# Performance work log

Measured on AMD Instinct MI355X. Metric: run time of the kernel, lower is better.

## Reference

```python
import jax, jax.numpy as jnp
import numpy as np

N_ATOMS = 30000
N_PAIRS = 1200000
N_BASIS = 7
N_RADIAL = 5
N_SPECIES = 119
R_MIN = 0.5
R_MAX = 6.0
UNITS = (512, 512)
BOX = 6.0  # Angstrom box edge so many pairs fall inside the cutoff
N_FEAT = 360  # gaussian-moment feature count for n_radial=5

# static triangular index sets (fully symmetric contractions)
_TRI2_I, _TRI2_J = np.triu_indices(N_RADIAL)
_TRI3 = np.array([(i, j, k) for i in range(N_RADIAL)
                  for j in range(i, N_RADIAL)
                  for k in range(j, N_RADIAL)], dtype=np.int32)


def setup_inputs() -> dict:
    key = jax.random.key(0)
    ks = jax.random.split(key, 8)
    R = jax.random.uniform(ks[0], (N_ATOMS, 3), jnp.float32) * BOX
    Z = jax.random.randint(ks[1], (N_ATOMS,), 0, N_SPECIES, dtype=jnp.int32)
    idx = jax.random.randint(ks[2], (2, N_PAIRS), 0, N_ATOMS, dtype=jnp.int32)
    W_radial = jax.random.normal(ks[3], (N_SPECIES, N_SPECIES, N_RADIAL, N_BASIS), jnp.float32) / np.sqrt(N_BASIS)
    w1 = jax.random.normal(ks[4], (N_FEAT, UNITS[0]), jnp.float32) / np.sqrt(N_FEAT)
    b1 = jnp.zeros((UNITS[0],), jnp.float32)
    w2 = jax.random.normal(ks[5], (UNITS[0], UNITS[1]), jnp.float32) / np.sqrt(UNITS[0])
    b2 = jnp.zeros((UNITS[1],), jnp.float32)
    w3 = jax.random.normal(ks[6], (UNITS[1], 1), jnp.float32) / np.sqrt(UNITS[1])
    b3 = jnp.zeros((1,), jnp.float32)
    scale = 2.0 * jnp.ones((N_SPECIES, 1), jnp.float32)
    shift = 1.0 * jnp.ones((N_SPECIES, 1), jnp.float32)
    return dict(R=R, Z=Z, idx=idx, W_radial=W_radial, w1=w1, b1=b1,
                w2=w2, b2=b2, w3=w3, b3=b3, scale=scale, shift=shift)


def _descriptor(R, Z, idx, W_radial):
    idx_i, idx_j = idx[0], idx[1]
    # pairwise displacement (free-space displacement fn)
    dr_vec = R[idx_j] - R[idx_i]                                  # [P,3]
    dr = jnp.sqrt(jnp.sum(dr_vec * dr_vec, axis=-1) + 1e-12)      # [P]
    dn = dr_vec / (dr + 1e-5)[:, None]                            # unit vectors [P,3]

    # gaussian radial basis
    betta = N_BASIS ** 2 / R_MAX ** 2
    rad_norm = (2.0 * betta / np.pi) ** 0.25
    shifts = R_MIN + (R_MAX - R_MIN) / N_BASIS * jnp.arange(N_BASIS, dtype=jnp.float32)
    basis = rad_norm * jnp.exp(-betta * (dr[:, None] - shifts) ** 2)  # [P,B]

    # cosine cutoff and per species-pair embedding of the basis
    cutoff = 0.5 * (jnp.cos(jnp.pi * dr / R_MAX) + 1.0) * (dr < R_MAX)
    coeffs = W_radial[Z[idx_i], Z[idx_j]]                          # [P,K,B] irregular gather
    radial = jnp.einsum('pkb,pb->pk', coeffs, basis)               # [P,K]
    radial = radial * (cutoff / np.sqrt(N_BASIS))[:, None]

    seg = lambda x: jax.ops.segment_sum(x, idx_i, num_segments=N_ATOMS)
    # geometric moments of order 0..3
    m0 = seg(radial)                                               # [A,K]
    m1 = seg(radial[:, :, None] * dn[:, None, :])                  # [A,K,3]
    dn2 = dn[:, :, None] * dn[:, None, :]                          # [P,3,3]
    m2 = seg(radial[:, :, None, None] * dn2[:, None])              # [A,K,3,3]
    dn3 = dn2[:, :, :, None] * dn[:, None, None, :]                # [P,3,3,3]
    m3 = seg(radial[:, :, None, None, None] * dn3[:, None])        # [A,K,3,3,3]

    # gaussian-moment invariant contractions
    c1 = jnp.einsum('ari,asi->ars', m1, m1)
    c2 = jnp.einsum('arij,asij->ars', m2, m2)
    c3 = jnp.einsum('arijk,asijk->ars', m3, m3)
    c4 = jnp.einsum('arij,asik,atjk->arst', m2, m2, m2)
    c5 = jnp.einsum('ari,asj,atij->arst', m1, m1, m2)
    c6 = jnp.einsum('arijk,asijl,atkl->arst', m3, m3, m2)
    c7 = jnp.einsum('arijk,asij,atk->arst', m3, m2, m1)

    A = m0.shape[0]
    gm = jnp.concatenate([
        m0,
        c1[:, _TRI2_I, _TRI2_J],
        c2[:, _TRI2_I, _TRI2_J],
        c3[:, _TRI2_I, _TRI2_J],
        c4[:, _TRI3[:, 0], _TRI3[:, 1], _TRI3[:, 2]],
        c5[:, _TRI2_I, _TRI2_J, :].reshape(A, -1),
        c6[:, _TRI2_I, _TRI2_J, :].reshape(A, -1),
        c7.reshape(A, -1),
    ], axis=-1)                                                    # [A,360]
    return gm


def reference(R, Z, idx, W_radial, w1, b1, w2, b2, w3, b3, scale, shift):
    gm = _descriptor(R, Z, idx, W_radial)
    h = jax.nn.swish(gm @ w1 + b1)
    h = jax.nn.swish(h @ w2 + b2)
    h = h @ w3 + b3                                                # [A,1]
    return scale[Z] * h + shift[Z]
```

## Files before the change

kernel.cpp:

```cpp
#include <hip/hip_runtime.h>

#define NA      30000
#define MPAD    30080
#define NPAIRS  1200000
#define NB      7
#define NK      5
#define NSP     119
#define NFEAT   360
#define KP1     384
#define NU      512
#define WROW    36
#define MAXSLOT 120
#define PSTRIDE 128
#define NBK     118
#define BCAP    11520
#define PPB     4688
#define NTILE   235

#define BETTA      1.3611111111111112f
#define RADNORM    0.96481348f
#define SHIFT_STEP 0.7857142857142857f
#define PI_OVER_R  0.5235987755982988f
#define INV_SQRT7  0.3779644730092272f
#define RMAXV      6.0f

typedef __attribute__((ext_vector_type(8))) short bf16x8;
typedef __attribute__((ext_vector_type(4))) float f32x4;
typedef __attribute__((ext_vector_type(2))) float f32x2;

__device__ __forceinline__ unsigned short f2b(float x) {
    unsigned u = __float_as_uint(x);
    unsigned r = u + 0x7FFF + ((u >> 16) & 1);
    return (unsigned short)(r >> 16);
}

__global__ __launch_bounds__(256)
void k_part(const int* __restrict__ idx, const int* __restrict__ Z,
            int* __restrict__ gcur, int* __restrict__ part) {
    __shared__ int hist[NBK];
    __shared__ int base[NBK];
    int tid = threadIdx.x;
    for (int b = tid; b < NBK; b += 256) hist[b] = 0;
    __syncthreads();
    int p0 = blockIdx.x * PPB;
    int p1 = min(p0 + PPB, NPAIRS);
    for (int p = p0 + tid; p < p1; p += 256)
        atomicAdd(&hist[idx[p] >> 8], 1);
    __syncthreads();
    for (int b = tid; b < NBK; b += 256) {
        base[b] = atomicAdd(&gcur[b], hist[b]);
        hist[b] = 0;
    }
    __syncthreads();
    for (int p = p0 + tid; p < p1; p += 256) {
        int i = idx[p];
        int b = i >> 8;
        int j = idx[NPAIRS + p];
        int zj = Z[j];
        int off = base[b] + atomicAdd(&hist[b], 1);
        if (off < BCAP)
            part[b * BCAP + off] = ((i & 255) << 22) | (zj << 15) | j;
    }
}

__global__ __launch_bounds__(256)
void k_csr(const int* __restrict__ part, const int* __restrict__ gcnt,
           int* __restrict__ counts, int* __restrict__ plist) {
    __shared__ int lp[128 * MAXSLOT];
    __shared__ int lc[128];
    int tid = threadIdx.x;
    int lane = tid & 63, wave = tid >> 6;
    int w = blockIdx.x;
    int cb = w >> 1;
    int par = w & 1;
    for (int t = tid; t < 128; t += 256) lc[t] = 0;
    __syncthreads();
    int n = min(gcnt[cb], BCAP);
    for (int e = tid; e < n; e += 256) {
        int v = part[cb * BCAP + e];
        int iloc = v >> 22;
        if ((iloc >> 7) == par) {
            int i7 = iloc & 127;
            int r = atomicAdd(&lc[i7], 1);
            if (r < MAXSLOT) lp[i7 * MAXSLOT + r] = v & 0x3FFFFF;
        }
    }
    __syncthreads();
    for (int t = tid; t < 128; t += 256) {
        int a = w * 128 + t;
        if (a < NA) counts[a] = min(lc[t], MAXSLOT);
    }
    for (int rr = 0; rr < 32; rr++) {
        int row = wave * 32 + rr;
        int a = w * 128 + row;
        if (a < NA) {
            for (int c = lane; c < MAXSLOT; c += 64)
                plist[(size_t)a * PSTRIDE + c] = lp[row * MAXSLOT + c];
        }
    }
}

#define PREP_W   (NSP*NSP*WROW)
#define PREP_R   NA
#define PREP_W1  (NU*KP1)
#define PREP_W2  (NU*NU)
#define PREP_TOT (PREP_W + PREP_R + PREP_W1 + PREP_W2)
__global__ void k_prep(const float* __restrict__ W, const float* __restrict__ R,
                       const float* __restrict__ w1, const float* __restrict__ w2,
                       float* __restrict__ Wp, float* __restrict__ Rp,
                       unsigned short* __restrict__ w1T, unsigned short* __restrict__ w2T,
                       int* __restrict__ gcur, float* __restrict__ out) {
    int i = blockIdx.x * blockDim.x + threadIdx.x;
    if (i < 128) gcur[i] = 0;
    if (i < NA) out[i] = 0.f;
    if (i < PREP_W) {
        int row = i / WROW, e = i - row * WROW;
        Wp[i] = (e < NK * NB) ? W[row * (NK * NB) + e] : 0.f;
        return;
    }
    i -= PREP_W;
    if (i < PREP_R) {
        f32x4 v = {R[3*i], R[3*i+1], R[3*i+2], 0.f};
        *(f32x4*)&Rp[4*i] = v;
        return;
    }
    i -= PREP_R;
    if (i < PREP_W1) {
        int c = i / KP1, kp = i - c * KP1;
        w1T[i] = (kp < NFEAT) ? f2b(w1[kp * NU + c]) : (unsigned short)0;
        return;
    }
    i -= PREP_W1;
    if (i < PREP_W2) {
        int c = i >> 9, kp = i & 511;
        w2T[i] = f2b(w2[kp * NU + c]);
    }
}

__global__ __launch_bounds__(512, 2)
void k_momcon(const float* __restrict__ Rp, const int* __restrict__ Z,
              const float* __restrict__ Wp, const int* __restrict__ counts,
              const int* __restrict__ plist, unsigned short* __restrict__ gmB) {
    __shared__ float MS[100 * 65];
    int tid = threadIdx.x;
    int g = tid >> 3, q = tid & 7;
    int a0 = blockIdx.x * 64;
    int a = a0 + g;

    if (a < NA) {
        f32x4 ri = *(const f32x4*)&Rp[4*a];
        int Zi = Z[a];
        f32x2 acc[50];
#pragma unroll
        for (int u = 0; u < 50; u++) acc[u] = (f32x2){0.f, 0.f};
        int cnt = min(counts[a], MAXSLOT);
        const int* prow = plist + (size_t)a * PSTRIDE;

        for (int t = q; t < cnt; t += 8) {
            int pk = prow[t];
            int j  = pk & 0x7FFF;
            int Zj = (pk >> 15) & 0x7F;
            f32x4 rj = *(const f32x4*)&Rp[4*j];

            const f32x4* wrow = (const f32x4*)&Wp[(Zi * NSP + Zj) * WROW];
            f32x4 w4[9];
#pragma unroll
            for (int c = 0; c < 9; c++) w4[c] = wrow[c];
            const float* wf = (const float*)w4;

            float dx = rj.x - ri.x, dy = rj.y - ri.y, dz = rj.z - ri.z;
            float d2 = dx*dx + dy*dy + dz*dz + 1e-12f;
            float dr = sqrtf(d2);
            float inv = 1.0f / (dr + 1e-5f);
            float nx = dx*inv, ny = dy*inv, nz = dz*inv;

            float basis[NB];
#pragma unroll
            for (int b = 0; b < NB; b++) {
                float tt = dr - (0.5f + SHIFT_STEP * (float)b);
                basis[b] = RADNORM * __expf(-BETTA * tt * tt);
            }
            float cut = (dr < RMAXV) ? 0.5f * (__cosf(PI_OVER_R * dr) + 1.0f) : 0.0f;
            cut *= INV_SQRT7;
            float rad[NK];
#pragma unroll
            for (int k = 0; k < NK; k++) {
                float s = 0.f;
#pragma unroll
                for (int b = 0; b < NB; b++) s += wf[k*NB + b] * basis[b];
                rad[k] = s * cut;
            }
            float gg[20];
            gg[0] = 1.f; gg[1] = nx; gg[2] = ny; gg[3] = nz;
            gg[4] = nx*nx; gg[5] = nx*ny; gg[6] = nx*nz; gg[7] = ny*ny; gg[8] = ny*nz; gg[9] = nz*nz;
            gg[10] = gg[4]*nx; gg[11] = gg[4]*ny; gg[12] = gg[4]*nz; gg[13] = gg[5]*ny; gg[14] = gg[5]*nz;
            gg[15] = gg[6]*nz; gg[16] = gg[7]*ny; gg[17] = gg[7]*nz; gg[18] = gg[8]*nz; gg[19] = gg[9]*nz;
            f32x2 g2[10];
#pragma unroll
            for (int u = 0; u < 10; u++) g2[u] = (f32x2){gg[2*u], gg[2*u+1]};
#pragma unroll
            for (int k = 0; k < NK; k++) {
                f32x2 rk = (f32x2){rad[k], rad[k]};
#pragma unroll
                for (int u = 0; u < 10; u++)
                    acc[k*10 + u] += rk * g2[u];
            }
        }
#pragma unroll
        for (int u = 0; u < 50; u++) {
            f32x2 v = acc[u];
            double d = __builtin_bit_cast(double, v);
            d = __shfl_xor(d, 1);
            v += __builtin_bit_cast(f32x2, d);
            d = __builtin_bit_cast(double, v);
            d = __shfl_xor(d, 2);
            v += __builtin_bit_cast(f32x2, d);
            d = __builtin_bit_cast(double, v);
            d = __shfl_xor(d, 4);
            v += __builtin_bit_cast(f32x2, d);
            acc[u] = v;
        }
        if (q == 0) {
#pragma unroll
            for (int u = 0; u < 50; u++) {
                MS[(2*u)     * 65 + g] = acc[u].x;
                MS[(2*u + 1) * 65 + g] = acc[u].y;
            }
        }
    }
    __syncthreads();

    int lane = tid & 63, wave = tid >> 6;
    if (wave >= 4) return;
    int aB = a0 + lane;
    bool ok = (aB < NA);
    const int S2[3][3] = {{0,1,2},{1,3,4},{2,4,5}};
    const int S3[3][3][3] = {
        {{0,1,2},{1,3,4},{2,4,5}},
        {{1,3,4},{3,6,7},{4,7,8}},
        {{2,4,5},{4,7,8},{5,8,9}}
    };
    unsigned short* row = gmB + (size_t)aB * KP1;
#define LD(comp) MS[(comp) * 65 + lane]

    if (wave == 0) {
        if (ok) {
            for (int k = 0; k < 5; k++) row[k] = f2b(LD(k * 20));
        }
        int f = 5;
        for (int r = 0; r < 5; r++)
            for (int s = r; s < 5; s++) {
                float v = 0.f;
#pragma unroll
                for (int i = 0; i < 3; i++) v += LD(r*20+1+i) * LD(s*20+1+i);
                if (ok) row[f] = f2b(v);
                f++;
            }
        const float W2U[6] = {1,2,2,1,2,1};
        for (int r = 0; r < 5; r++)
            for (int s = r; s < 5; s++) {
                float v = 0.f;
#pragma unroll
                for (int u = 0; u < 6; u++) v += W2U[u] * LD(r*20+4+u) * LD(s*20+4+u);
                if (ok) row[f] = f2b(v);
                f++;
            }
        const float W3U[10] = {1,3,3,3,6,3,1,3,3,1};
        for (int r = 0; r < 5; r++)
            for (int s = r; s < 5; s++) {
                float v = 0.f;
#pragma unroll
                for (int u = 0; u < 10; u++) v += W3U[u] * LD(r*20+10+u) * LD(s*20+10+u);
                if (ok) row[f] = f2b(v);
                f++;
            }
        for (int r = 0; r < 5; r++) {
            float m2r[6];
#pragma unroll
            for (int u = 0; u < 6; u++) m2r[u] = LD(r*20+4+u);
            for (int s = r; s < 5; s++) {
                float m2q[6];
#pragma unroll
                for (int u = 0; u < 6; u++) m2q[u] = LD(s*20+4+u);
                for (int t = s; t < 5; t++) {
                    float m2t[6];
#pragma unroll
                    for (int u = 0; u < 6; u++) m2t[u] = LD(t*20+4+u);
                    float v = 0.f;
#pragma unroll
                    for (int i = 0; i < 3; i++)
#pragma unroll
                        for (int j = 0; j < 3; j++)
#pragma unroll
                            for (int k = 0; k < 3; k++)
                                v += m2r[S2[i][j]] * m2q[S2[i][k]] * m2t[S2[j][k]];
                    if (ok) row[f] = f2b(v);
                    f++;
                }
            }
        }
    } else if (wave == 1) {
        int f = 85;
        for (int r = 0; r < 5; r++) {
            float m1r[3];
#pragma unroll
            for (int i = 0; i < 3; i++) m1r[i] = LD(r*20+1+i);
            for (int s = r; s < 5; s++) {
                float m1q[3];
#pragma unroll
                for (int i = 0; i < 3; i++) m1q[i] = LD(s*20+1+i);
                for (int t = 0; t < 5; t++) {
                    float m2t[6];
#pragma unroll
                    for (int u = 0; u < 6; u++) m2t[u] = LD(t*20+4+u);
                    float v = 0.f;
#pragma unroll
                    for (int i = 0; i < 3; i++)
#pragma unroll
                        for (int j = 0; j < 3; j++)
                            v += m1r[i] * m1q[j] * m2t[S2[i][j]];
                    if (ok) row[f] = f2b(v);
                    f++;
                }
            }
        }
        f = 235;
        for (int r = 0; r < 5; r++) {
            float m3r[10];
#pragma unroll
            for (int u = 0; u < 10; u++) m3r[u] = LD(r*20+10+u);
            for (int s = 0; s < 5; s++) {
                float m2q[6];
#pragma unroll
                for (int u = 0; u < 6; u++) m2q[u] = LD(s*20+4+u);
                float U0 = 0.f, U1 = 0.f, U2 = 0.f;
#pragma unroll
                for (int i = 0; i < 3; i++)
#pragma unroll
                    for (int j = 0; j < 3; j++) {
                        float ww = m2q[S2[i][j]];
                        U0 += m3r[S3[i][j][0]] * ww;
                        U1 += m3r[S3[i][j][1]] * ww;
                        U2 += m3r[S3[i][j][2]] * ww;
                    }
                for (int t = 0; t < 5; t++) {
                    float v = U0 * LD(t*20+1) + U1 * LD(t*20+2) + U2 * LD(t*20+3);
                    if (ok) row[f] = f2b(v);
                    f++;
                }
            }
        }
    } else {
        int pbeg = (wave == 2) ? 0 : 7;
        int pend = (wave == 2) ? 7 : 15;
        int p = 0;
        for (int r = 0; r < 5; r++)
            for (int s = r; s < 5; s++) {
                if (p >= pbeg && p < pend) {
                    float m3r[10], m3q[10];
#pragma unroll
                    for (int u = 0; u < 10; u++) m3r[u] = LD(r*20+10+u);
#pragma unroll
                    for (int u = 0; u < 10; u++) m3q[u] = LD(s*20+10+u);
                    float T[3][3];
#pragma unroll
                    for (int k = 0; k < 3; k++)
#pragma unroll
                        for (int l = 0; l < 3; l++) {
                            float v = 0.f;
#pragma unroll
                            for (int i = 0; i < 3; i++)
#pragma unroll
                                for (int j = 0; j < 3; j++)
                                    v += m3r[S3[i][j][k]] * m3q[S3[i][j][l]];
                            T[k][l] = v;
                        }
                    int f = 160 + p * 5;
                    for (int t = 0; t < 5; t++) {
                        float m2t[6];
#pragma unroll
                        for (int u = 0; u < 6; u++) m2t[u] = LD(t*20+4+u);
                        float v = 0.f;
#pragma unroll
                        for (int k = 0; k < 3; k++)
#pragma unroll
                            for (int l = 0; l < 3; l++)
                                v += T[k][l] * m2t[S2[k][l]];
                        if (ok) row[f + t] = f2b(v);
                    }
                }
                p++;
            }
        if (wave == 3 && ok) {
            for (int z = NFEAT; z < KP1; z++) row[z] = 0;
        }
    }
#undef LD
}

__device__ __forceinline__ void stage8(const unsigned short* gp, unsigned short* lp) {
    __builtin_amdgcn_global_load_lds(
        (const __attribute__((address_space(1))) unsigned int*)gp,
        (__attribute__((address_space(3))) unsigned int*)lp, 16, 0, 0);
}

template<int KPAD, int MODE>
__global__ __launch_bounds__(256) void k_mfma(const unsigned short* __restrict__ A,
                                              const unsigned short* __restrict__ B,
                                              const float* __restrict__ bias,
                                              const float* __restrict__ w3,
                                              void* __restrict__ outp) {
    __shared__ __align__(16) unsigned char SMEM[35072];
    unsigned short* As = (unsigned short*)SMEM;
    unsigned short* Bs = (unsigned short*)(SMEM + 16384);
    float* red = (float*)(SMEM + 32768);
    int tid = threadIdx.x;
    int lane = tid & 63, wave = tid >> 6;
    int wm = wave >> 1, wn = wave & 1;
    int quad = lane >> 4, l16 = lane & 15;
    int lrow = lane >> 3;
    int lchk = lane & 7;

    for (int t = 0; t < 2; t++) {
        int atile = blockIdx.y * 2 + t;
        if (atile >= NTILE) break;
        int rowA0, rowB0;
        if (MODE == 1) { rowA0 = atile * 128;      rowB0 = blockIdx.x * 128; }
        else           { rowA0 = blockIdx.x * 128; rowB0 = atile * 128; }

        f32x4 acc[4][4];
        f32x4 zero = {0.f, 0.f, 0.f, 0.f};
#pragma unroll
        for (int i = 0; i < 4; i++)
#pragma unroll
            for (int j = 0; j < 4; j++) acc[i][j] = zero;

        for (int k0 = 0; k0 < KPAD; k0 += 64) {
            __syncthreads();
#pragma unroll
            for (int i = 0; i < 4; i++) {
                int r = wave * 32 + i * 8 + lrow;
                int gc = lchk ^ (r & 7);
                stage8(A + (size_t)(rowA0 + r) * KPAD + k0 + gc * 8, &As[(wave * 32 + i * 8) * 64]);
            }
#pragma unroll
            for (int i = 0; i < 4; i++) {
                int r = wave * 32 + i * 8 + lrow;
                int gc = lchk ^ (r & 7);
                stage8(B + (size_t)(rowB0 + r) * KPAD + k0 + gc * 8, &Bs[(wave * 32 + i * 8) * 64]);
            }
            __syncthreads();
#pragma unroll
            for (int s = 0; s < 2; s++) {
                bf16x8 af[4], bfr[4];
#pragma unroll
                for (int mt = 0; mt < 4; mt++) {
                    int r = wm * 64 + mt * 16 + l16;
                    af[mt] = *(const bf16x8*)&As[r * 64 + (((s * 4 + quad) ^ (r & 7)) * 8)];
                }
#pragma unroll
                for (int nt = 0; nt < 4; nt++) {
                    int r = wn * 64 + nt * 16 + l16;
                    bfr[nt] = *(const bf16x8*)&Bs[r * 64 + (((s * 4 + quad) ^ (r & 7)) * 8)];
                }
#pragma unroll
                for (int mt = 0; mt < 4; mt++)
#pragma unroll
                    for (int nt = 0; nt < 4; nt++)
                        acc[mt][nt] = __builtin_amdgcn_mfma_f32_16x16x32_bf16(
                            af[mt], bfr[nt], acc[mt][nt], 0, 0, 0);
            }
        }

        if (MODE == 1) {
            __syncthreads();
            unsigned short* Ot = (unsigned short*)SMEM;
#pragma unroll
            for (int nt = 0; nt < 4; nt++) {
                int c_loc = wn * 64 + nt * 16 + l16;
                float b = bias[rowB0 + c_loc];
#pragma unroll
                for (int mt = 0; mt < 4; mt++) {
#pragma unroll
                    for (int reg = 0; reg < 4; reg++) {
                        int a_loc = wm * 64 + mt * 16 + quad * 4 + reg;
                        float v = acc[mt][nt][reg] + b;
                        Ot[a_loc * 136 + c_loc] = f2b(v / (1.f + __expf(-v)));
                    }
                }
            }
            __syncthreads();
            unsigned short* O = (unsigned short*)outp;
            int half = lane >> 5, l32 = lane & 31;
#pragma unroll
            for (int it = 0; it < 16; it++) {
                int rloc = wave * 32 + it * 2 + half;
                int a = rowA0 + rloc;
                unsigned long long d = *(const unsigned long long*)&Ot[rloc * 136 + l32 * 4];
                if (a < NA)
                    *(unsigned long long*)&O[(size_t)a * NU + rowB0 + l32 * 4] = d;
            }
        } else {
            float pn[4] = {0.f, 0.f, 0.f, 0.f};
#pragma unroll
            for (int mt = 0; mt < 4; mt++) {
#pragma unroll
                for (int reg = 0; reg < 4; reg++) {
                    int c = rowA0 + wm * 64 + mt * 16 + quad * 4 + reg;
                    float b = bias[c];
                    float w3c = w3[c];
#pragma unroll
                    for (int nt = 0; nt < 4; nt++) {
                        float v = acc[mt][nt][reg] + b;
                        pn[nt] += w3c * (v / (1.f + __expf(-v)));
                    }
                }
            }
#pragma unroll
            for (int nt = 0; nt < 4; nt++) {
                pn[nt] += __shfl_xor(pn[nt], 16);
                pn[nt] += __shfl_xor(pn[nt], 32);
            }
            __syncthreads();
            if (quad == 0) {
#pragma unroll
                for (int nt = 0; nt < 4; nt++)
                    red[((wm * 2 + wn) * 4 + nt) * 16 + l16] = pn[nt];
            }
            __syncthreads();
            if (tid < 128) {
                int wn2 = tid >> 6, nt2 = (tid >> 4) & 3, lb = tid & 15;
                float s = red[((0 * 2 + wn2) * 4 + nt2) * 16 + lb]
                        + red[((1 * 2 + wn2) * 4 + nt2) * 16 + lb];
                int a = rowB0 + wn2 * 64 + nt2 * 16 + lb;
                if (a < NA) atomicAdd((float*)outp + a, s);
            }
        }
    }
}

__global__ void k_finish(float* __restrict__ out, const float* __restrict__ b3,
                         const int* __restrict__ Z, const float* __restrict__ scale,
                         const float* __restrict__ shift) {
    int a = blockIdx.x * blockDim.x + threadIdx.x;
    if (a >= NA) return;
    int z = Z[a];
    out[a] = scale[z] * (out[a] + b3[0]) + shift[z];
}

extern "C" void kernel_launch(void* const* d_in, const int* in_sizes, int n_in,
                              void* d_out, int out_size, void* d_ws, size_t ws_size,
                              hipStream_t stream) {
    const float* R    = (const float*)d_in[0];
    const int*   Z    = (const int*)  d_in[1];
    const int*   idx  = (const int*)  d_in[2];
    const float* Wr   = (const float*)d_in[3];
    const float* w1   = (const float*)d_in[4];
    const float* b1   = (const float*)d_in[5];
    const float* w2   = (const float*)d_in[6];
    const float* b2   = (const float*)d_in[7];
    const float* w3   = (const float*)d_in[8];
    const float* b3   = (const float*)d_in[9];
    const float* scale= (const float*)d_in[10];
    const float* shift= (const float*)d_in[11];
    float* out = (float*)d_out;
    char* ws = (char*)d_ws;

    int*            gcur   = (int*)  (ws + 0);
    int*            counts = (int*)  (ws + 512);
    int*            part   = (int*)  (ws + 120576);
    int*            plist  = (int*)  (ws + 5558016);
    unsigned short* gmB    = (unsigned short*)(ws + 32918016);
    unsigned short* w1T    = (unsigned short*)(ws + 56019456);
    unsigned short* w2T    = (unsigned short*)(ws + 56412672);
    unsigned short* h1B    = (unsigned short*)(ws + 56936960);
    float*          Wpad   = (float*)(ws + 87738880);
    float*          Rpad   = (float*)(ws + 89778064);

    k_prep   <<<(PREP_TOT + 255) / 256, 256, 0, stream>>>(Wr, R, w1, w2, Wpad, Rpad,
                                                          w1T, w2T, gcur, out);
    k_part   <<<256, 256, 0, stream>>>(idx, Z, gcur, part);
    k_csr    <<<235, 256, 0, stream>>>(part, gcur, counts, plist);
    k_momcon <<<(NA + 63) / 64, 512, 0, stream>>>(Rpad, Z, Wpad, counts, plist, gmB);

    k_mfma<KP1, 1><<<dim3(NU / 128, 118), 256, 0, stream>>>(gmB, w1T, b1, nullptr, (void*)h1B);
    k_mfma<NU,  2><<<dim3(NU / 128, 118), 256, 0, stream>>>(w2T, h1B, b2, w3, (void*)out);

    k_finish<<<(NA + 255) / 256, 256, 0, stream>>>(out, b3, Z, scale, shift);
}
```

Measured before the change: 257.5 us.

## Spread moment contractions across all eight waves and stage output rows in LDS

The invariant-contraction phase of the moment kernel used to run on only four of its eight waves, and each lane wrote scattered 2-byte values straight to global memory. Now all eight waves share a rebalanced set of c4/c5/c6/c7 contractions. Results go into a shared-memory staging buffer and are copied out as coalesced 4-byte stores, in two passes that reuse the buffer. The cost is extra LDS (about 31 KB), which may limit occupancy, and extra block-wide barriers.

```diff
diff --git a/kernel.cpp b/kernel.cpp
--- a/kernel.cpp
+++ b/kernel.cpp
@@ -137,11 +137,111 @@
     }
 }
 
+#define LDM(comp) M[(comp) * 65]
+
+__device__ __forceinline__ void do_c5(const float* M, unsigned short* STrow,
+                                      int r, int s, int foff) {
+    const int S2[3][3] = {{0,1,2},{1,3,4},{2,4,5}};
+    float m1r[3], m1q[3];
+#pragma unroll
+    for (int i = 0; i < 3; i++) m1r[i] = LDM(r*20+1+i);
+#pragma unroll
+    for (int i = 0; i < 3; i++) m1q[i] = LDM(s*20+1+i);
+    float pre[9];
+#pragma unroll
+    for (int i = 0; i < 3; i++)
+#pragma unroll
+        for (int j = 0; j < 3; j++) pre[i*3+j] = m1r[i] * m1q[j];
+    for (int t = 0; t < 5; t++) {
+        float m2t[6];
+#pragma unroll
+        for (int u = 0; u < 6; u++) m2t[u] = LDM(t*20+4+u);
+        float v = 0.f;
+#pragma unroll
+        for (int i = 0; i < 3; i++)
+#pragma unroll
+            for (int j = 0; j < 3; j++)
+                v += pre[i*3+j] * m2t[S2[i][j]];
+        STrow[foff + t] = f2b(v);
+    }
+}
+
+__device__ __forceinline__ void do_c6(const float* M, unsigned short* STrow,
+                                      int r, int s, int foff) {
+    const int S2[3][3] = {{0,1,2},{1,3,4},{2,4,5}};
+    const int S3[3][3][3] = {
+        {{0,1,2},{1,3,4},{2,4,5}},
+        {{1,3,4},{3,6,7},{4,7,8}},
+        {{2,4,5},{4,7,8},{5,8,9}}
+    };
+    float m3r[10];
+#pragma unroll
+    for (int u = 0; u < 10; u++) m3r[u] = LDM(r*20+10+u);
+    float m2q[6];
+#pragma unroll
+    for (int u = 0; u < 6; u++) m2q[u] = LDM(s*20+4+u);
+    float U0 = 0.f, U1 = 0.f, U2 = 0.f;
+#pragma unroll
+    for (int i = 0; i < 3; i++)
+#pragma unroll
+        for (int j = 0; j < 3; j++) {
+            float ww = m2q[S2[i][j]];
+            U0 += m3r[S3[i][j][0]] * ww;
+            U1 += m3r[S3[i][j][1]] * ww;
+            U2 += m3r[S3[i][j][2]] * ww;
+        }
+    for (int t = 0; t < 5; t++) {
+        float v = U0 * LDM(t*20+1) + U1 * LDM(t*20+2) + U2 * LDM(t*20+3);
+        STrow[foff + t] = f2b(v);
+    }
+}
+
+__device__ __forceinline__ void do_c7(const float* M, unsigned short* STrow,
+                                      int r, int s, int foff) {
+    const int S2[3][3] = {{0,1,2},{1,3,4},{2,4,5}};
+    const int S3[3][3][3] = {
+        {{0,1,2},{1,3,4},{2,4,5}},
+        {{1,3,4},{3,6,7},{4,7,8}},
+        {{2,4,5},{4,7,8},{5,8,9}}
+    };
+    float m3r[10], m3q[10];
+#pragma unroll
+    for (int u = 0; u < 10; u++) m3r[u] = LDM(r*20+10+u);
+#pragma unroll
+    for (int u = 0; u < 10; u++) m3q[u] = LDM(s*20+10+u);
+    float T[3][3];
+#pragma unroll
+    for (int k = 0; k < 3; k++)
+#pragma unroll
+        for (int l = 0; l < 3; l++) {
+            float v = 0.f;
+#pragma unroll
+            for (int i = 0; i < 3; i++)
+#pragma unroll
+                for (int j = 0; j < 3; j++)
+                    v += m3r[S3[i][j][k]] * m3q[S3[i][j][l]];
+            T[k][l] = v;
+        }
+    for (int t = 0; t < 5; t++) {
+        float m2t[6];
+#pragma unroll
+        for (int u = 0; u < 6; u++) m2t[u] = LDM(t*20+4+u);
+        float v = 0.f;
+#pragma unroll
+        for (int k = 0; k < 3; k++)
+#pragma unroll
+            for (int l = 0; l < 3; l++)
+                v += T[k][l] * m2t[S2[k][l]];
+        STrow[foff + t] = f2b(v);
+    }
+}
+
 __global__ __launch_bounds__(512, 2)
 void k_momcon(const float* __restrict__ Rp, const int* __restrict__ Z,
               const float* __restrict__ Wp, const int* __restrict__ counts,
               const int* __restrict__ plist, unsigned short* __restrict__ gmB) {
     __shared__ float MS[100 * 65];
+    __shared__ __align__(4) unsigned short ST[64 * 242];
     int tid = threadIdx.x;
     int g = tid >> 3, q = tid & 7;
     int a0 = blockIdx.x * 64;
@@ -231,171 +331,116 @@
     __syncthreads();
 
     int lane = tid & 63, wave = tid >> 6;
-    if (wave >= 4) return;
-    int aB = a0 + lane;
-    bool ok = (aB < NA);
-    const int S2[3][3] = {{0,1,2},{1,3,4},{2,4,5}};
-    const int S3[3][3][3] = {
-        {{0,1,2},{1,3,4},{2,4,5}},
-        {{1,3,4},{3,6,7},{4,7,8}},
-        {{2,4,5},{4,7,8},{5,8,9}}
-    };
-    unsigned short* row = gmB + (size_t)aB * KP1;
-#define LD(comp) MS[(comp) * 65 + lane]
+    const float* M = MS + lane;
+    unsigned short* STrow = ST + lane * 242;
 
     if (wave == 0) {
-        if (ok) {
-            for (int k = 0; k < 5; k++) row[k] = f2b(LD(k * 20));
-        }
+        for (int k = 0; k < 5; k++) STrow[k] = f2b(LDM(k * 20));
         int f = 5;
         for (int r = 0; r < 5; r++)
             for (int s = r; s < 5; s++) {
                 float v = 0.f;
 #pragma unroll
-                for (int i = 0; i < 3; i++) v += LD(r*20+1+i) * LD(s*20+1+i);
-                if (ok) row[f] = f2b(v);
-                f++;
+                for (int i = 0; i < 3; i++) v += LDM(r*20+1+i) * LDM(s*20+1+i);
+                STrow[f++] = f2b(v);
             }
         const float W2U[6] = {1,2,2,1,2,1};
         for (int r = 0; r < 5; r++)
             for (int s = r; s < 5; s++) {
                 float v = 0.f;
 #pragma unroll
-                for (int u = 0; u < 6; u++) v += W2U[u] * LD(r*20+4+u) * LD(s*20+4+u);
-                if (ok) row[f] = f2b(v);
-                f++;
+                for (int u = 0; u < 6; u++) v += W2U[u] * LDM(r*20+4+u) * LDM(s*20+4+u);
+                STrow[f++] = f2b(v);
             }
         const float W3U[10] = {1,3,3,3,6,3,1,3,3,1};
         for (int r = 0; r < 5; r++)
             for (int s = r; s < 5; s++) {
                 float v = 0.f;
 #pragma unroll
-                for (int u = 0; u < 10; u++) v += W3U[u] * LD(r*20+10+u) * LD(s*20+10+u);
-                if (ok) row[f] = f2b(v);
-                f++;
-            }
-        for (int r = 0; r < 5; r++) {
-            float m2r[6];
-#pragma unroll
-            for (int u = 0; u < 6; u++) m2r[u] = LD(r*20+4+u);
-            for (int s = r; s < 5; s++) {
-                float m2q[6];
-#pragma unroll
-                for (int u = 0; u < 6; u++) m2q[u] = LD(s*20+4+u);
+                for (int u = 0; u < 10; u++) v += W3U[u] * LDM(r*20+10+u) * LDM(s*20+10+u);
+                STrow[f++] = f2b(v);
+            }
+        do_c7(M, STrow, 3, 4, 160 + 13*5);
+        do_c7(M, STrow, 4, 4, 160 + 14*5);
+    } else if (wave == 1 || wave == 2) {
+        const int S2[3][3] = {{0,1,2},{1,3,4},{2,4,5}};
+        int e0 = (wave == 1) ? 0 : 18, e1 = (wave == 1) ? 18 : 35;
+        int e = 0;
+        for (int r = 0; r < 5; r++)
+            for (int s = r; s < 5; s++)
                 for (int t = s; t < 5; t++) {
-                    float m2t[6];
-#pragma unroll
-                    for (int u = 0; u < 6; u++) m2t[u] = LD(t*20+4+u);
-                    float v = 0.f;
-#pragma unroll
-                    for (int i = 0; i < 3; i++)
-#pragma unroll
-                        for (int j = 0; j < 3; j++)
-#pragma unroll
-                            for (int k = 0; k < 3; k++)
-                                v += m2r[S2[i][j]] * m2q[S2[i][k]] * m2t[S2[j][k]];
-                    if (ok) row[f] = f2b(v);
-                    f++;
+                    if (e >= e0 && e < e1) {
+                        float m2r[6], m2q[6], m2t[6];
+#pragma unroll
+                        for (int u = 0; u < 6; u++) m2r[u] = LDM(r*20+4+u);
+#pragma unroll
+                        for (int u = 0; u < 6; u++) m2q[u] = LDM(s*20+4+u);
+#pragma unroll
+                        for (int u = 0; u < 6; u++) m2t[u] = LDM(t*20+4+u);
+                        float v = 0.f;
+#pragma unroll
+                        for (int i = 0; i < 3; i++)
+#pragma unroll
+                            for (int j = 0; j < 3; j++)
+#pragma unroll
+                                for (int k = 0; k < 3; k++)
+                                    v += m2r[S2[i][j]] * m2q[S2[i][k]] * m2t[S2[j][k]];
+                        STrow[50 + e] = f2b(v);
+                    }
+                    e++;
                 }
-            }
-        }
-    } else if (wave == 1) {
-        int f = 85;
-        for (int r = 0; r < 5; r++) {
-            float m1r[3];
-#pragma unroll
-            for (int i = 0; i < 3; i++) m1r[i] = LD(r*20+1+i);
-            for (int s = r; s < 5; s++) {
-                float m1q[3];
-#pragma unroll
-                for (int i = 0; i < 3; i++) m1q[i] = LD(s*20+1+i);
-                for (int t = 0; t < 5; t++) {
-                    float m2t[6];
-#pragma unroll
-                    for (int u = 0; u < 6; u++) m2t[u] = LD(t*20+4+u);
-                    float v = 0.f;
-#pragma unroll
-                    for (int i = 0; i < 3; i++)
-#pragma unroll
-                        for (int j = 0; j < 3; j++)
-                            v += m1r[i] * m1q[j] * m2t[S2[i][j]];
-                    if (ok) row[f] = f2b(v);
-                    f++;
-                }
-            }
-        }
-        f = 235;
-        for (int r = 0; r < 5; r++) {
-            float m3r[10];
-#pragma unroll
-            for (int u = 0; u < 10; u++) m3r[u] = LD(r*20+10+u);
-            for (int s = 0; s < 5; s++) {
-                float m2q[6];
-#pragma unroll
-                for (int u = 0; u < 6; u++) m2q[u] = LD(s*20+4+u);
-                float U0 = 0.f, U1 = 0.f, U2 = 0.f;
-#pragma unroll
-                for (int i = 0; i < 3; i++)
-#pragma unroll
-                    for (int j = 0; j < 3; j++) {
-                        float ww = m2q[S2[i][j]];
-                        U0 += m3r[S3[i][j][0]] * ww;
-                        U1 += m3r[S3[i][j][1]] * ww;
-                        U2 += m3r[S3[i][j][2]] * ww;
-                    }
-                for (int t = 0; t < 5; t++) {
-                    float v = U0 * LD(t*20+1) + U1 * LD(t*20+2) + U2 * LD(t*20+3);
-                    if (ok) row[f] = f2b(v);
-                    f++;
-                }
-            }
-        }
-    } else {
-        int pbeg = (wave == 2) ? 0 : 7;
-        int pend = (wave == 2) ? 7 : 15;
+    } else if (wave == 3) {
         int p = 0;
         for (int r = 0; r < 5; r++)
             for (int s = r; s < 5; s++) {
-                if (p >= pbeg && p < pend) {
-                    float m3r[10], m3q[10];
-#pragma unroll
-                    for (int u = 0; u < 10; u++) m3r[u] = LD(r*20+10+u);
-#pragma unroll
-                    for (int u = 0; u < 10; u++) m3q[u] = LD(s*20+10+u);
-                    float T[3][3];
-#pragma unroll
-                    for (int k = 0; k < 3; k++)
-#pragma unroll
-                        for (int l = 0; l < 3; l++) {
-                            float v = 0.f;
-#pragma unroll
-                            for (int i = 0; i < 3; i++)
-#pragma unroll
-                                for (int j = 0; j < 3; j++)
-                                    v += m3r[S3[i][j][k]] * m3q[S3[i][j][l]];
-                            T[k][l] = v;
-                        }
-                    int f = 160 + p * 5;
-                    for (int t = 0; t < 5; t++) {
-                        float m2t[6];
-#pragma unroll
-                        for (int u = 0; u < 6; u++) m2t[u] = LD(t*20+4+u);
-                        float v = 0.f;
-#pragma unroll
-                        for (int k = 0; k < 3; k++)
-#pragma unroll
-                            for (int l = 0; l < 3; l++)
-                                v += T[k][l] * m2t[S2[k][l]];
-                        if (ok) row[f + t] = f2b(v);
-                    }
-                }
+                if (p < 8) do_c5(M, STrow, r, s, 85 + p*5);
                 p++;
             }
-        if (wave == 3 && ok) {
-            for (int z = NFEAT; z < KP1; z++) row[z] = 0;
-        }
-    }
-#undef LD
+        do_c7(M, STrow, 3, 3, 160 + 12*5);
+    } else if (wave == 4) {
+        int p = 0;
+        for (int r = 0; r < 5; r++)
+            for (int s = r; s < 5; s++) {
+                if (p >= 8) do_c5(M, STrow, r, s, 85 + p*5);
+                p++;
+            }
+        do_c6(M, STrow, 0, 0, 235);
+    } else {
+        int pc0 = (wave - 5) * 4;
+        int p = 0;
+        for (int r = 0; r < 5; r++)
+            for (int s = r; s < 5; s++) {
+                if (p >= pc0 && p < pc0 + 4) do_c7(M, STrow, r, s, 160 + p*5);
+                p++;
+            }
+    }
+    __syncthreads();
+    for (int e = tid; e < 64 * 120; e += 512) {
+        int row = e / 120, c = e - row * 120;
+        if (a0 + row < NA)
+            *(unsigned int*)&gmB[(size_t)(a0 + row) * KP1 + 2*c] =
+                *(const unsigned int*)&ST[row * 242 + 2*c];
+    }
+    __syncthreads();
+
+    {
+        int g0 = 1 + wave * 3;
+        for (int gi = 0; gi < 3; gi++) {
+            int gr = g0 + gi;
+            int r = gr / 5, s = gr - r * 5;
+            do_c6(M, STrow, r, s, 235 + gr*5 - 240);
+        }
+        if (wave == 0) {
+            for (int z = 360; z < 384; z++) STrow[z - 240] = 0;
+        }
+    }
+    __syncthreads();
+    for (int e = tid; e < 64 * 72; e += 512) {
+        int row = e / 72, c = e - row * 72;
+        if (a0 + row < NA)
+            *(unsigned int*)&gmB[(size_t)(a0 + row) * KP1 + 240 + 2*c] =
+                *(const unsigned int*)&ST[row * 242 + 2*c];
+    }
 }
 
 __device__ __forceinline__ void stage8(const unsigned short* gp, unsigned short* lp) {
```

Measured after the change: 256.7 us. No clear change (-0.3%).
